# Optimization experiments

Measured on AMD Instinct MI355X. Metric: run time of the kernel, lower is better.

Reference implementation:

```python
import jax, jax.numpy as jnp
import numpy as np

C, C_H, N_HEAD = 8, 1, 8
B, S, I = 1, 4096, 1024


def setup_inputs() -> dict:
    key = jax.random.key(0)
    ks = jax.random.split(key, 8)
    m = jax.random.normal(ks[0], (B, S, I, C), dtype=jnp.float32)
    mask = jnp.ones((B, S, I), dtype=jnp.float32)
    sc = 0.1
    return {
        "m": m,
        "mask": mask,
        "ln_gamma": jnp.ones((C,), jnp.float32),
        "ln_beta": jnp.zeros((C,), jnp.float32),
        "Wq": jax.random.normal(ks[1], (C, C_H * N_HEAD), jnp.float32) * sc,
        "Wk": jax.random.normal(ks[2], (C, C_H), jnp.float32) * sc,
        "Wv": jax.random.normal(ks[3], (C, C_H), jnp.float32) * sc,
        "Wg": jax.random.normal(ks[4], (C, C_H * N_HEAD), jnp.float32) * sc,
        "bg": jax.random.normal(ks[5], (C_H * N_HEAD,), jnp.float32) * sc,
        "Wo": jax.random.normal(ks[6], (C_H * N_HEAD, C), jnp.float32) * sc,
        "bo": jax.random.normal(ks[7], (C,), jnp.float32) * sc,
    }


def reference(m, mask, ln_gamma, ln_beta, Wq, Wk, Wv, Wg, bg, Wo, bo):
    # m: (B, s, i, c) -> work in (B, i, s, c); mask: (B, s, i) -> (B, i, s)
    mt = jnp.swapaxes(m, -2, -3)
    mk = jnp.swapaxes(mask, -1, -2)
    c_h = Wk.shape[1]
    h = Wq.shape[1] // c_h
    Bz, iz, sz, _ = mt.shape

    # LayerNorm over channel dim (eps=1e-5, population variance)
    mu = jnp.mean(mt, axis=-1, keepdims=True)
    var = jnp.mean(jnp.square(mt - mu), axis=-1, keepdims=True)
    mn = (mt - mu) / jnp.sqrt(var + 1e-5) * ln_gamma + ln_beta  # (B,i,s,c)

    # Masked mean pool over sequences -> global query per residue column
    q = jnp.sum(mn * mk[..., None], axis=-2) / (jnp.sum(mk, axis=-1)[..., None] + 1e-5)  # (B,i,c)

    q = (q @ Wq) * (c_h ** -0.5)          # (B,i,h*c_h)
    k = mn @ Wk                           # (B,i,s,c_h)  shared across heads
    v = mn @ Wv                           # (B,i,s,c_h)
    g = jax.nn.sigmoid(mn @ Wg + bg)      # (B,i,s,h*c_h)

    q = q.reshape(Bz, iz, h, c_h)
    g = g.reshape(Bz, iz, sz, h, c_h)

    bias = 1e9 * (mk - 1.0)               # (B,i,s)
    a = jnp.einsum('bihd,bisd->bihs', q, k) + bias[..., None, :]
    a = jax.nn.softmax(a, axis=-1)        # (B,i,h,s)
    o = jnp.einsum('bihs,bisd->bihd', a, v)  # (B,i,h,c_h)

    o = o[..., None, :, :] * g            # (B,i,s,h,c_h) gated, broadcast over s
    o = o.reshape(Bz, iz, sz, h * c_h) @ Wo + bo  # (B,i,s,c)
    return jnp.swapaxes(o, -2, -3)        # (B,s,i,c)
```

## Files before the change

kernel.cpp:

```cpp
#include <hip/hip_runtime.h>

#define I_LEN 1024
#define S_LEN 4096

typedef float f32x4 __attribute__((ext_vector_type(4)));

__device__ __forceinline__ unsigned int f2h(float f) {
  _Float16 h = (_Float16)f; unsigned short u;
  __builtin_memcpy(&u, &h, 2); return (unsigned int)u;
}
__device__ __forceinline__ float h2f(unsigned int u) {
  unsigned short s = (unsigned short)u; _Float16 h;
  __builtin_memcpy(&h, &s, 2); return (float)h;
}

__global__ __launch_bounds__(256, 2) void msa_k1a(
    const float* __restrict__ m, const float* __restrict__ mask,
    const float* __restrict__ lng, const float* __restrict__ lnb,
    const float* __restrict__ Wk, const float* __restrict__ Wv,
    const float* __restrict__ Wg, const float* __restrict__ bg,
    unsigned int* __restrict__ kvS, uint4* __restrict__ glS,
    float* __restrict__ qpart)
{
  const int b  = blockIdx.x;
  const int cg = b & 15;
  const int sb = b >> 4;
  const int t  = threadIdx.x;
  const int w  = t >> 6;
  const int l  = t & 63;
  const int i  = cg * 64 + w * 16 + (l & 15);
  const int sg = l >> 4;
  const int s0 = sb * 32 + sg * 8;

  float swk = 0.f, swv = 0.f, kb = 0.f, vb = 0.f;
  float sgv[8], tbv[8];
#pragma unroll
  for (int c = 0; c < 8; ++c) {
    swk = fmaf(lng[c], Wk[c], swk);  swv = fmaf(lng[c], Wv[c], swv);
    kb  = fmaf(lnb[c], Wk[c], kb);   vb  = fmaf(lnb[c], Wv[c], vb);
  }
#pragma unroll
  for (int h = 0; h < 8; ++h) {
    float sv_ = 0.f, tb = bg[h];
#pragma unroll
    for (int c = 0; c < 8; ++c) {
      sv_ = fmaf(lng[c], Wg[c * 8 + h], sv_);
      tb  = fmaf(lnb[c], Wg[c * 8 + h], tb);
    }
    sgv[h] = sv_; tbv[h] = tb;
  }

  float qnx[8] = {0,0,0,0,0,0,0,0};
  float qd = 0.f;

#pragma unroll
  for (int half = 0; half < 2; ++half) {
    float4 L[4], H[4]; float MK[4];
#pragma unroll
    for (int r = 0; r < 4; ++r) {
      const int s = s0 + half * 4 + r;
      const size_t base = (size_t)(s * I_LEN + i);
      const float4* mp = (const float4*)(m + base * 8);
      L[r] = mp[0]; H[r] = mp[1];
      MK[r] = mask[base];
    }
#pragma unroll
    for (int r = 0; r < 4; ++r) {
      const int s = s0 + half * 4 + r;
      const size_t base = (size_t)(s * I_LEN + i);
      float x[8] = {L[r].x, L[r].y, L[r].z, L[r].w, H[r].x, H[r].y, H[r].z, H[r].w};
      const float mk = MK[r];
      float su = 0.f, s2 = 0.f;
#pragma unroll
      for (int c = 0; c < 8; ++c) { su += x[c]; s2 = fmaf(x[c], x[c], s2); }
      const float mu   = su * 0.125f;
      const float var  = s2 * 0.125f - mu * mu;
      const float rstd = rsqrtf(var + 1e-5f);
      float dk = 0.f, dv = 0.f;
#pragma unroll
      for (int c = 0; c < 8; ++c) {
        const float xg = x[c] * lng[c];
        dk = fmaf(xg, Wk[c], dk);
        dv = fmaf(xg, Wv[c], dv);
        x[c] = xg;
      }
      const float kk = fmaf(rstd, fmaf(-mu, swk, dk), kb);
      const float vv = fmaf(rstd, fmaf(-mu, swv, dv), vb);

      unsigned int gw[4];
#pragma unroll
      for (int j = 0; j < 4; ++j) {
        float d0 = 0.f, d1 = 0.f;
#pragma unroll
        for (int c = 0; c < 8; ++c) {
          d0 = fmaf(x[c], Wg[c * 8 + 2 * j],     d0);
          d1 = fmaf(x[c], Wg[c * 8 + 2 * j + 1], d1);
        }
        const float gl0 = fmaf(rstd, fmaf(-mu, sgv[2 * j],     d0), tbv[2 * j]);
        const float gl1 = fmaf(rstd, fmaf(-mu, sgv[2 * j + 1], d1), tbv[2 * j + 1]);
        const float g0 = 65535.f / (1.0f + __expf(-gl0));
        const float g1 = 65535.f / (1.0f + __expf(-gl1));
        const unsigned int u0 = (unsigned int)__float2int_rn(g0);
        const unsigned int u1 = (unsigned int)__float2int_rn(g1);
        gw[j] = u0 | (u1 << 16);
      }
      glS[base] = make_uint4(gw[0], gw[1], gw[2], gw[3]);
      kvS[base] = (mk > 0.5f) ? ((f2h(kk) << 16) | f2h(vv)) : 0xFFFFFFFFu;

      const float mr  = mk * rstd;
      const float mmr = -mu * mr;
#pragma unroll
      for (int c = 0; c < 8; ++c)
        qnx[c] = fmaf(x[c], mr, fmaf(lng[c], mmr, qnx[c]));
      qd += mk;
    }
  }

  float red[9];
#pragma unroll
  for (int q = 0; q < 9; ++q) {
    float x = (q < 8) ? qnx[q] : qd;
    x += __shfl_xor(x, 16);
    x += __shfl_xor(x, 32);
    red[q] = x;
  }
  if (l < 16) {
    float4* pp = (float4*)(qpart + ((size_t)sb * I_LEN + i) * 12);
    pp[0] = make_float4(red[0], red[1], red[2], red[3]);
    pp[1] = make_float4(red[4], red[5], red[6], red[7]);
    pp[2] = make_float4(red[8], 0.f, 0.f, 0.f);
  }
}

__global__ __launch_bounds__(64) void msa_k1b(
    const float* __restrict__ lnb, const float* __restrict__ Wq,
    const float* __restrict__ qpart, float* __restrict__ qtab)
{
  const int l  = threadIdx.x;
  const int i  = blockIdx.x * 4 + (l & 3);
  const int sl = l >> 2;
  float acc[9] = {0,0,0,0,0,0,0,0,0};
#pragma unroll
  for (int it = 0; it < 8; ++it) {
    const int sb = sl + it * 16;
    const float4* p = (const float4*)(qpart + ((size_t)sb * I_LEN + i) * 12);
    const float4 a = p[0], b4 = p[1], c4 = p[2];
    acc[0] += a.x;  acc[1] += a.y;  acc[2] += a.z;  acc[3] += a.w;
    acc[4] += b4.x; acc[5] += b4.y; acc[6] += b4.z; acc[7] += b4.w;
    acc[8] += c4.x;
  }
#pragma unroll
  for (int q = 0; q < 9; ++q) {
    float x = acc[q];
    x += __shfl_xor(x, 4);
    x += __shfl_xor(x, 8);
    x += __shfl_xor(x, 16);
    x += __shfl_xor(x, 32);
    acc[q] = x;
  }
  if (l < 4) {
    const float d   = acc[8];
    const float inv = 1.0f / (d + 1e-5f);
    float qs[8];
#pragma unroll
    for (int c = 0; c < 8; ++c) qs[c] = (acc[c] + lnb[c] * d) * inv;
    float qv[8];
#pragma unroll
    for (int h = 0; h < 8; ++h) {
      float v = 0.f;
#pragma unroll
      for (int c = 0; c < 8; ++c) v = fmaf(qs[c], Wq[c * 8 + h], v);
      qv[h] = v;
    }
    float4* qp = (float4*)(qtab + (size_t)i * 8);
    qp[0] = make_float4(qv[0], qv[1], qv[2], qv[3]);
    qp[1] = make_float4(qv[4], qv[5], qv[6], qv[7]);
  }
}

__global__ __launch_bounds__(256, 2) void msa_k1c(
    const unsigned int* __restrict__ kvS, const float* __restrict__ qtab,
    float* __restrict__ spart)
{
  const int b  = blockIdx.x;
  const int cg = b & 15;
  const int sb = b >> 4;
  const int t  = threadIdx.x;
  const int w  = t >> 6;
  const int l  = t & 63;
  const int i  = cg * 64 + w * 16 + (l & 15);
  const int sg = l >> 4;
  const int s0 = sb * 32 + sg * 8;

  const float4* qp = (const float4*)(qtab + (size_t)i * 8);
  const float4 q0 = qp[0], q1 = qp[1];
  const float qh[8] = {q0.x, q0.y, q0.z, q0.w, q1.x, q1.y, q1.z, q1.w};

  float se[8] = {0,0,0,0,0,0,0,0};
  float sv[8] = {0,0,0,0,0,0,0,0};
#pragma unroll
  for (int half = 0; half < 2; ++half) {
    unsigned int W[4];
#pragma unroll
    for (int r = 0; r < 4; ++r)
      W[r] = kvS[(size_t)((s0 + half * 4 + r) * I_LEN + i)];
#pragma unroll
    for (int r = 0; r < 4; ++r) {
      const unsigned int wv = W[r];
      const bool on = (wv != 0xFFFFFFFFu);
      const float kk = h2f(wv >> 16);
      const float vv = h2f(wv & 0xFFFFu);
#pragma unroll
      for (int h = 0; h < 8; ++h) {
        const float e = on ? __expf(qh[h] * kk) : 0.0f;
        se[h] += e;
        sv[h] = fmaf(e, vv, sv[h]);
      }
    }
  }
  float red[16];
#pragma unroll
  for (int q = 0; q < 16; ++q) {
    float x = (q < 8) ? se[q] : sv[q - 8];
    x += __shfl_xor(x, 16);
    x += __shfl_xor(x, 32);
    red[q] = x;
  }
  if (l < 16) {
    float4* pp = (float4*)(spart + ((size_t)sb * I_LEN + i) * 16);
    pp[0] = make_float4(red[0],  red[1],  red[2],  red[3]);
    pp[1] = make_float4(red[4],  red[5],  red[6],  red[7]);
    pp[2] = make_float4(red[8],  red[9],  red[10], red[11]);
    pp[3] = make_float4(red[12], red[13], red[14], red[15]);
  }
}

__global__ __launch_bounds__(64) void msa_k1d(
    const float* __restrict__ spart, float* __restrict__ o_tab)
{
  const int l  = threadIdx.x;
  const int i  = blockIdx.x * 4 + (l & 3);
  const int sl = l >> 2;
  float acc[16] = {0,0,0,0,0,0,0,0,0,0,0,0,0,0,0,0};
#pragma unroll
  for (int it = 0; it < 8; ++it) {
    const int sb = sl + it * 16;
    const float4* p = (const float4*)(spart + ((size_t)sb * I_LEN + i) * 16);
    const float4 a = p[0], b4 = p[1], c4 = p[2], d4 = p[3];
    acc[0]  += a.x;  acc[1]  += a.y;  acc[2]  += a.z;  acc[3]  += a.w;
    acc[4]  += b4.x; acc[5]  += b4.y; acc[6]  += b4.z; acc[7]  += b4.w;
    acc[8]  += c4.x; acc[9]  += c4.y; acc[10] += c4.z; acc[11] += c4.w;
    acc[12] += d4.x; acc[13] += d4.y; acc[14] += d4.z; acc[15] += d4.w;
  }
#pragma unroll
  for (int q = 0; q < 16; ++q) {
    float x = acc[q];
    x += __shfl_xor(x, 4);
    x += __shfl_xor(x, 8);
    x += __shfl_xor(x, 16);
    x += __shfl_xor(x, 32);
    acc[q] = x;
  }
  if (l < 4) {
    float4* op = (float4*)(o_tab + (size_t)i * 8);
    op[0] = make_float4(acc[8]  / acc[0], acc[9]  / acc[1],
                        acc[10] / acc[2], acc[11] / acc[3]);
    op[1] = make_float4(acc[12] / acc[4], acc[13] / acc[5],
                        acc[14] / acc[6], acc[15] / acc[7]);
  }
}

__global__ __launch_bounds__(256, 2) void msa_k2(
    const uint4* __restrict__ glS, const float* __restrict__ o_tab,
    const float* __restrict__ Wo, const float* __restrict__ bo,
    float* __restrict__ out)
{
  const int tid = blockIdx.x * 256 + threadIdx.x;
  const int i = tid & (I_LEN - 1);

  const float4* op = (const float4*)(o_tab + (size_t)i * 8);
  const float4 o1 = op[0], o2 = op[1];
  const float kfx = 1.0f / 65535.f;
  const float A[8] = {o1.x * kfx, o1.y * kfx, o1.z * kfx, o1.w * kfx,
                      o2.x * kfx, o2.y * kfx, o2.z * kfx, o2.w * kfx};

#pragma unroll 2
  for (int q = 0; q < 8; ++q) {
    const size_t p = (size_t)tid + (size_t)q * 524288;
    const uint4 G = glS[p];
    const unsigned int gw[4] = {G.x, G.y, G.z, G.w};
    float acc[8];
#pragma unroll
    for (int c = 0; c < 8; ++c) acc[c] = bo[c];
#pragma unroll
    for (int j = 0; j < 4; ++j) {
      const float gv0 = A[2 * j]     * (float)(gw[j] & 0xFFFFu);
      const float gv1 = A[2 * j + 1] * (float)(gw[j] >> 16);
#pragma unroll
      for (int c = 0; c < 8; ++c) {
        acc[c] = fmaf(gv0, Wo[(2 * j) * 8 + c], acc[c]);
        acc[c] = fmaf(gv1, Wo[(2 * j + 1) * 8 + c], acc[c]);
      }
    }
    f32x4* outp = (f32x4*)(out + p * 8);
    f32x4 r0 = {acc[0], acc[1], acc[2], acc[3]};
    f32x4 r1 = {acc[4], acc[5], acc[6], acc[7]};
    __builtin_nontemporal_store(r0, outp);
    __builtin_nontemporal_store(r1, outp + 1);
  }
}

extern "C" void kernel_launch(void* const* d_in, const int* in_sizes, int n_in,
                              void* d_out, int out_size, void* d_ws, size_t ws_size,
                              hipStream_t stream) {
  const float* m    = (const float*)d_in[0];
  const float* mask = (const float*)d_in[1];
  const float* lng  = (const float*)d_in[2];
  const float* lnb  = (const float*)d_in[3];
  const float* Wq   = (const float*)d_in[4];
  const float* Wk   = (const float*)d_in[5];
  const float* Wv   = (const float*)d_in[6];
  const float* Wg   = (const float*)d_in[7];
  const float* bg   = (const float*)d_in[8];
  const float* Wo   = (const float*)d_in[9];
  const float* bo   = (const float*)d_in[10];
  float* out = (float*)d_out;

  char* ws = (char*)d_ws;
  float*        o_tab = (float*)ws;
  float*        qtab  = (float*)(ws + ((size_t)64 << 10));
  unsigned int* kvS   = (unsigned int*)(ws + ((size_t)1 << 20));
  uint4*        glS   = (uint4*)(ws + ((size_t)32 << 20));
  float*        qpart = (float*)(ws + ((size_t)104 << 20));
  float*        spart = (float*)(ws + ((size_t)112 << 20));

  hipLaunchKernelGGL(msa_k1a, dim3(2048), dim3(256), 0, stream,
                     m, mask, lng, lnb, Wk, Wv, Wg, bg, kvS, glS, qpart);
  hipLaunchKernelGGL(msa_k1b, dim3(256), dim3(64), 0, stream,
                     lnb, Wq, qpart, qtab);
  hipLaunchKernelGGL(msa_k1c, dim3(2048), dim3(256), 0, stream,
                     kvS, qtab, spart);
  hipLaunchKernelGGL(msa_k1d, dim3(256), dim3(64), 0, stream,
                     spart, o_tab);
  hipLaunchKernelGGL(msa_k2, dim3(2048), dim3(256), 0, stream,
                     glS, o_tab, Wo, bo, out);
}
```

Baseline: 331.0 us.

## Recompute LayerNorm and gates in output kernel instead of storing gate buffer

Measured after the change: 328.8 us. About the same (-0.6%).

```diff
diff --git a/kernel.cpp b/kernel.cpp
--- a/kernel.cpp
+++ b/kernel.cpp
@@ -18,9 +18,7 @@
     const float* __restrict__ m, const float* __restrict__ mask,
     const float* __restrict__ lng, const float* __restrict__ lnb,
     const float* __restrict__ Wk, const float* __restrict__ Wv,
-    const float* __restrict__ Wg, const float* __restrict__ bg,
-    unsigned int* __restrict__ kvS, uint4* __restrict__ glS,
-    float* __restrict__ qpart)
+    unsigned int* __restrict__ kvS, float* __restrict__ qpart)
 {
   const int b  = blockIdx.x;
   const int cg = b & 15;
@@ -33,87 +31,53 @@
   const int s0 = sb * 32 + sg * 8;
 
   float swk = 0.f, swv = 0.f, kb = 0.f, vb = 0.f;
-  float sgv[8], tbv[8];
 #pragma unroll
   for (int c = 0; c < 8; ++c) {
     swk = fmaf(lng[c], Wk[c], swk);  swv = fmaf(lng[c], Wv[c], swv);
     kb  = fmaf(lnb[c], Wk[c], kb);   vb  = fmaf(lnb[c], Wv[c], vb);
   }
-#pragma unroll
-  for (int h = 0; h < 8; ++h) {
-    float sv_ = 0.f, tb = bg[h];
-#pragma unroll
-    for (int c = 0; c < 8; ++c) {
-      sv_ = fmaf(lng[c], Wg[c * 8 + h], sv_);
-      tb  = fmaf(lnb[c], Wg[c * 8 + h], tb);
-    }
-    sgv[h] = sv_; tbv[h] = tb;
-  }
+
+  float4 L[8], H[8]; float MK[8];
+#pragma unroll
+  for (int r = 0; r < 8; ++r) {
+    const size_t base = (size_t)((s0 + r) * I_LEN + i);
+    const float4* mp = (const float4*)(m + base * 8);
+    L[r] = mp[0]; H[r] = mp[1];
+    MK[r] = mask[base];
+  }
+  __builtin_amdgcn_sched_barrier(0);
 
   float qnx[8] = {0,0,0,0,0,0,0,0};
   float qd = 0.f;
-
-#pragma unroll
-  for (int half = 0; half < 2; ++half) {
-    float4 L[4], H[4]; float MK[4];
-#pragma unroll
-    for (int r = 0; r < 4; ++r) {
-      const int s = s0 + half * 4 + r;
-      const size_t base = (size_t)(s * I_LEN + i);
-      const float4* mp = (const float4*)(m + base * 8);
-      L[r] = mp[0]; H[r] = mp[1];
-      MK[r] = mask[base];
-    }
-#pragma unroll
-    for (int r = 0; r < 4; ++r) {
-      const int s = s0 + half * 4 + r;
-      const size_t base = (size_t)(s * I_LEN + i);
-      float x[8] = {L[r].x, L[r].y, L[r].z, L[r].w, H[r].x, H[r].y, H[r].z, H[r].w};
-      const float mk = MK[r];
-      float su = 0.f, s2 = 0.f;
-#pragma unroll
-      for (int c = 0; c < 8; ++c) { su += x[c]; s2 = fmaf(x[c], x[c], s2); }
-      const float mu   = su * 0.125f;
-      const float var  = s2 * 0.125f - mu * mu;
-      const float rstd = rsqrtf(var + 1e-5f);
-      float dk = 0.f, dv = 0.f;
-#pragma unroll
-      for (int c = 0; c < 8; ++c) {
-        const float xg = x[c] * lng[c];
-        dk = fmaf(xg, Wk[c], dk);
-        dv = fmaf(xg, Wv[c], dv);
-        x[c] = xg;
-      }
-      const float kk = fmaf(rstd, fmaf(-mu, swk, dk), kb);
-      const float vv = fmaf(rstd, fmaf(-mu, swv, dv), vb);
-
-      unsigned int gw[4];
-#pragma unroll
-      for (int j = 0; j < 4; ++j) {
-        float d0 = 0.f, d1 = 0.f;
-#pragma unroll
-        for (int c = 0; c < 8; ++c) {
-          d0 = fmaf(x[c], Wg[c * 8 + 2 * j],     d0);
-          d1 = fmaf(x[c], Wg[c * 8 + 2 * j + 1], d1);
-        }
-        const float gl0 = fmaf(rstd, fmaf(-mu, sgv[2 * j],     d0), tbv[2 * j]);
-        const float gl1 = fmaf(rstd, fmaf(-mu, sgv[2 * j + 1], d1), tbv[2 * j + 1]);
-        const float g0 = 65535.f / (1.0f + __expf(-gl0));
-        const float g1 = 65535.f / (1.0f + __expf(-gl1));
-        const unsigned int u0 = (unsigned int)__float2int_rn(g0);
-        const unsigned int u1 = (unsigned int)__float2int_rn(g1);
-        gw[j] = u0 | (u1 << 16);
-      }
-      glS[base] = make_uint4(gw[0], gw[1], gw[2], gw[3]);
-      kvS[base] = (mk > 0.5f) ? ((f2h(kk) << 16) | f2h(vv)) : 0xFFFFFFFFu;
-
-      const float mr  = mk * rstd;
-      const float mmr = -mu * mr;
-#pragma unroll
-      for (int c = 0; c < 8; ++c)
-        qnx[c] = fmaf(x[c], mr, fmaf(lng[c], mmr, qnx[c]));
-      qd += mk;
-    }
+#pragma unroll
+  for (int r = 0; r < 8; ++r) {
+    const size_t base = (size_t)((s0 + r) * I_LEN + i);
+    float x[8] = {L[r].x, L[r].y, L[r].z, L[r].w, H[r].x, H[r].y, H[r].z, H[r].w};
+    const float mk = MK[r];
+    float su = 0.f, s2 = 0.f;
+#pragma unroll
+    for (int c = 0; c < 8; ++c) { su += x[c]; s2 = fmaf(x[c], x[c], s2); }
+    const float mu   = su * 0.125f;
+    const float var  = s2 * 0.125f - mu * mu;
+    const float rstd = rsqrtf(var + 1e-5f);
+    float dk = 0.f, dv = 0.f;
+#pragma unroll
+    for (int c = 0; c < 8; ++c) {
+      const float xg = x[c] * lng[c];
+      dk = fmaf(xg, Wk[c], dk);
+      dv = fmaf(xg, Wv[c], dv);
+      x[c] = xg;
+    }
+    const float kk = fmaf(rstd, fmaf(-mu, swk, dk), kb);
+    const float vv = fmaf(rstd, fmaf(-mu, swv, dv), vb);
+    kvS[base] = (mk > 0.5f) ? ((f2h(kk) << 16) | f2h(vv)) : 0xFFFFFFFFu;
+
+    const float mr  = mk * rstd;
+    const float mmr = -mu * mr;
+#pragma unroll
+    for (int c = 0; c < 8; ++c)
+      qnx[c] = fmaf(x[c], mr, fmaf(lng[c], mmr, qnx[c]));
+    qd += mk;
   }
 
   float red[9];
@@ -196,26 +160,25 @@
   const float4 q0 = qp[0], q1 = qp[1];
   const float qh[8] = {q0.x, q0.y, q0.z, q0.w, q1.x, q1.y, q1.z, q1.w};
 
+  unsigned int W[8];
+#pragma unroll
+  for (int r = 0; r < 8; ++r)
+    W[r] = kvS[(size_t)((s0 + r) * I_LEN + i)];
+  __builtin_amdgcn_sched_barrier(0);
+
   float se[8] = {0,0,0,0,0,0,0,0};
   float sv[8] = {0,0,0,0,0,0,0,0};
 #pragma unroll
-  for (int half = 0; half < 2; ++half) {
-    unsigned int W[4];
-#pragma unroll
-    for (int r = 0; r < 4; ++r)
-      W[r] = kvS[(size_t)((s0 + half * 4 + r) * I_LEN + i)];
-#pragma unroll
-    for (int r = 0; r < 4; ++r) {
-      const unsigned int wv = W[r];
-      const bool on = (wv != 0xFFFFFFFFu);
-      const float kk = h2f(wv >> 16);
-      const float vv = h2f(wv & 0xFFFFu);
-#pragma unroll
-      for (int h = 0; h < 8; ++h) {
-        const float e = on ? __expf(qh[h] * kk) : 0.0f;
-        se[h] += e;
-        sv[h] = fmaf(e, vv, sv[h]);
-      }
+  for (int r = 0; r < 8; ++r) {
+    const unsigned int wv = W[r];
+    const bool on = (wv != 0xFFFFFFFFu);
+    const float kk = h2f(wv >> 16);
+    const float vv = on ? h2f(wv & 0xFFFFu) : 0.0f;
+#pragma unroll
+    for (int h = 0; h < 8; ++h) {
+      const float e = on ? __expf(qh[h] * kk) : 0.0f;
+      se[h] += e;
+      sv[h] = fmaf(e, vv, sv[h]);
     }
   }
   float red[16];
@@ -271,42 +234,73 @@
 }
 
 __global__ __launch_bounds__(256, 2) void msa_k2(
-    const uint4* __restrict__ glS, const float* __restrict__ o_tab,
+    const float* __restrict__ m,
+    const float* __restrict__ lng, const float* __restrict__ lnb,
+    const float* __restrict__ Wg, const float* __restrict__ bg,
     const float* __restrict__ Wo, const float* __restrict__ bo,
-    float* __restrict__ out)
+    const float* __restrict__ o_tab, float* __restrict__ out)
 {
   const int tid = blockIdx.x * 256 + threadIdx.x;
   const int i = tid & (I_LEN - 1);
 
+  float sgv[8], tbv[8];
+#pragma unroll
+  for (int h = 0; h < 8; ++h) {
+    float s = 0.f, tb = bg[h];
+#pragma unroll
+    for (int c = 0; c < 8; ++c) {
+      s  = fmaf(lng[c], Wg[c * 8 + h], s);
+      tb = fmaf(lnb[c], Wg[c * 8 + h], tb);
+    }
+    sgv[h] = s; tbv[h] = tb;
+  }
+
   const float4* op = (const float4*)(o_tab + (size_t)i * 8);
   const float4 o1 = op[0], o2 = op[1];
-  const float kfx = 1.0f / 65535.f;
-  const float A[8] = {o1.x * kfx, o1.y * kfx, o1.z * kfx, o1.w * kfx,
-                      o2.x * kfx, o2.y * kfx, o2.z * kfx, o2.w * kfx};
-
-#pragma unroll 2
-  for (int q = 0; q < 8; ++q) {
-    const size_t p = (size_t)tid + (size_t)q * 524288;
-    const uint4 G = glS[p];
-    const unsigned int gw[4] = {G.x, G.y, G.z, G.w};
-    float acc[8];
-#pragma unroll
-    for (int c = 0; c < 8; ++c) acc[c] = bo[c];
-#pragma unroll
-    for (int j = 0; j < 4; ++j) {
-      const float gv0 = A[2 * j]     * (float)(gw[j] & 0xFFFFu);
-      const float gv1 = A[2 * j + 1] * (float)(gw[j] >> 16);
-#pragma unroll
-      for (int c = 0; c < 8; ++c) {
-        acc[c] = fmaf(gv0, Wo[(2 * j) * 8 + c], acc[c]);
-        acc[c] = fmaf(gv1, Wo[(2 * j + 1) * 8 + c], acc[c]);
+  const float A[8] = {o1.x, o1.y, o1.z, o1.w, o2.x, o2.y, o2.z, o2.w};
+
+#pragma unroll
+  for (int g2 = 0; g2 < 2; ++g2) {
+    float4 LO[4], HI[4];
+#pragma unroll
+    for (int r = 0; r < 4; ++r) {
+      const size_t p = (size_t)tid + (size_t)(g2 * 4 + r) * 524288;
+      const float4* mp = (const float4*)(m + p * 8);
+      LO[r] = mp[0]; HI[r] = mp[1];
+    }
+    __builtin_amdgcn_sched_barrier(0);
+#pragma unroll
+    for (int r = 0; r < 4; ++r) {
+      const size_t p = (size_t)tid + (size_t)(g2 * 4 + r) * 524288;
+      float x[8] = {LO[r].x, LO[r].y, LO[r].z, LO[r].w,
+                    HI[r].x, HI[r].y, HI[r].z, HI[r].w};
+      float su = 0.f, s2 = 0.f;
+#pragma unroll
+      for (int c = 0; c < 8; ++c) { su += x[c]; s2 = fmaf(x[c], x[c], s2); }
+      const float mu   = su * 0.125f;
+      const float var  = s2 * 0.125f - mu * mu;
+      const float rstd = rsqrtf(var + 1e-5f);
+#pragma unroll
+      for (int c = 0; c < 8; ++c) x[c] *= lng[c];
+      float acc[8];
+#pragma unroll
+      for (int c = 0; c < 8; ++c) acc[c] = bo[c];
+#pragma unroll
+      for (int h = 0; h < 8; ++h) {
+        float d = 0.f;
+#pragma unroll
+        for (int c = 0; c < 8; ++c) d = fmaf(x[c], Wg[c * 8 + h], d);
+        const float gl = fmaf(rstd, fmaf(-mu, sgv[h], d), tbv[h]);
+        const float gv = A[h] / (1.0f + __expf(-gl));
+#pragma unroll
+        for (int c = 0; c < 8; ++c) acc[c] = fmaf(gv, Wo[h * 8 + c], acc[c]);
       }
-    }
-    f32x4* outp = (f32x4*)(out + p * 8);
-    f32x4 r0 = {acc[0], acc[1], acc[2], acc[3]};
-    f32x4 r1 = {acc[4], acc[5], acc[6], acc[7]};
-    __builtin_nontemporal_store(r0, outp);
-    __builtin_nontemporal_store(r1, outp + 1);
+      f32x4* outp = (f32x4*)(out + p * 8);
+      f32x4 r0 = {acc[0], acc[1], acc[2], acc[3]};
+      f32x4 r1 = {acc[4], acc[5], acc[6], acc[7]};
+      __builtin_nontemporal_store(r0, outp);
+      __builtin_nontemporal_store(r1, outp + 1);
+    }
   }
 }
 
@@ -330,12 +324,11 @@
   float*        o_tab = (float*)ws;
   float*        qtab  = (float*)(ws + ((size_t)64 << 10));
   unsigned int* kvS   = (unsigned int*)(ws + ((size_t)1 << 20));
-  uint4*        glS   = (uint4*)(ws + ((size_t)32 << 20));
-  float*        qpart = (float*)(ws + ((size_t)104 << 20));
-  float*        spart = (float*)(ws + ((size_t)112 << 20));
+  float*        qpart = (float*)(ws + ((size_t)32 << 20));
+  float*        spart = (float*)(ws + ((size_t)48 << 20));
 
   hipLaunchKernelGGL(msa_k1a, dim3(2048), dim3(256), 0, stream,
-                     m, mask, lng, lnb, Wk, Wv, Wg, bg, kvS, glS, qpart);
+                     m, mask, lng, lnb, Wk, Wv, kvS, qpart);
   hipLaunchKernelGGL(msa_k1b, dim3(256), dim3(64), 0, stream,
                      lnb, Wq, qpart, qtab);
   hipLaunchKernelGGL(msa_k1c, dim3(2048), dim3(256), 0, stream,
@@ -343,5 +336,5 @@
   hipLaunchKernelGGL(msa_k1d, dim3(256), dim3(64), 0, stream,
                      spart, o_tab);
   hipLaunchKernelGGL(msa_k2, dim3(2048), dim3(256), 0, stream,
-                     glS, o_tab, Wo, bo, out);
-}
+                     m, lng, lnb, Wg, bg, Wo, bo, o_tab, out);
+}
```
